# Performance work log

Measured on AMD Instinct MI355X. Metric: run time of the kernel, lower is better.

## Reference

```python
import jax, jax.numpy as jnp
import numpy as np

B, S, FC, FO = 16, 512, 24, 16
D, H, DK, FF, L = 512, 8, 64, 2048, 4
MAXPOS = 512
EPS = 1e-6


def _ln(x, scale, bias):
    mu = jnp.mean(x, axis=-1, keepdims=True)
    var = jnp.mean((x - mu) ** 2, axis=-1, keepdims=True)
    return (x - mu) * jax.lax.rsqrt(var + EPS) * scale + bias


def setup_inputs() -> dict:
    key = jax.random.key(0)
    ks = iter(jax.random.split(key, 64))
    def rn(shape, s=0.02):
        return (jax.random.normal(next(ks), shape, dtype=jnp.float32) * s)
    inp = {
        'x_cgm': jax.random.normal(next(ks), (B, S, FC), dtype=jnp.float32),
        'x_other': jax.random.normal(next(ks), (B, FO), dtype=jnp.float32),
        'cgm_W': rn((FC, D)), 'cgm_b': jnp.zeros((D,), jnp.float32),
        'rel_emb': rn((2 * MAXPOS - 1, DK)),
        'Wq': rn((L, D, H * DK)), 'bq': jnp.zeros((L, H * DK), jnp.float32),
        'Wk': rn((L, D, H * DK)), 'bk': jnp.zeros((L, H * DK), jnp.float32),
        'Wv': rn((L, D, H * DK)), 'bv': jnp.zeros((L, H * DK), jnp.float32),
        'Wo': rn((L, H * DK, D)), 'bo': jnp.zeros((L, D), jnp.float32),
        'Wg': rn((L, D, D)), 'bg': jnp.zeros((L, D), jnp.float32),
        'Wf1': rn((L, D, FF)), 'bf1': jnp.zeros((L, FF), jnp.float32),
        'Wfg': rn((L, D, FF)), 'bfg': jnp.zeros((L, FF), jnp.float32),
        'Wf2': rn((L, FF, D)), 'bf2': jnp.zeros((L, D), jnp.float32),
        'ln1_s': jnp.ones((L, D), jnp.float32), 'ln1_b': jnp.zeros((L, D), jnp.float32),
        'ln2_s': jnp.ones((L, D), jnp.float32), 'ln2_b': jnp.zeros((L, D), jnp.float32),
        'other_W': rn((FO, D)), 'other_b': jnp.zeros((D,), jnp.float32),
        'fW1': rn((2 * D, 256)), 'fb1': jnp.zeros((256,), jnp.float32),
        'fln1_s': jnp.ones((256,), jnp.float32), 'fln1_b': jnp.zeros((256,), jnp.float32),
        'fW2': rn((256, 128)), 'fb2': jnp.zeros((128,), jnp.float32),
        'fln2_s': jnp.ones((128,), jnp.float32), 'fln2_b': jnp.zeros((128,), jnp.float32),
        'fW3': rn((128, 1)), 'fb3': jnp.zeros((1,), jnp.float32),
    }
    return inp


def reference(x_cgm, x_other, cgm_W, cgm_b, rel_emb, Wq, bq, Wk, bk, Wv, bv,
              Wo, bo, Wg, bg, Wf1, bf1, Wfg, bfg, Wf2, bf2,
              ln1_s, ln1_b, ln2_s, ln2_b, other_W, other_b,
              fW1, fb1, fln1_s, fln1_b, fW2, fb2, fln2_s, fln2_b, fW3, fb3):
    x = x_cgm @ cgm_W + cgm_b  # [B,S,D]
    # relative position bias: rel_emb[i-j+MAXPOS-1] -> [S,S,DK], reduced by mean over depth
    idx = jnp.arange(S)
    pos_idx = idx[:, None] - idx[None, :] + MAXPOS - 1
    pos_bias = jnp.mean(rel_emb[pos_idx], axis=-1)  # [S,S]
    scale = jnp.sqrt(jnp.float32(DK))
    for l in range(L):
        q = (x @ Wq[l] + bq[l]).reshape(B, S, H, DK)
        k = (x @ Wk[l] + bk[l]).reshape(B, S, H, DK)
        v = (x @ Wv[l] + bv[l]).reshape(B, S, H, DK)
        scores = jnp.einsum('bqhd,bkhd->bhqk', q, k) / scale + pos_bias  # [B,H,S,S]
        probs = jax.nn.softmax(scores, axis=-1)
        ctx = jnp.einsum('bhqk,bkhd->bqhd', probs, v).reshape(B, S, H * DK)
        att = ctx @ Wo[l] + bo[l]
        gate = jax.nn.sigmoid(x @ Wg[l] + bg[l])
        x = _ln(x + gate * att, ln1_s[l], ln1_b[l])
        ff = (x @ Wf1[l] + bf1[l]) * jax.nn.sigmoid(x @ Wfg[l] + bfg[l])
        ff = ff @ Wf2[l] + bf2[l]
        x = _ln(x + ff, ln2_s[l], ln2_b[l])
    x = jnp.mean(x, axis=1)  # [B,D]
    xo = x_other @ other_W + other_b
    h = jnp.concatenate([x, xo], axis=-1)  # [B,2D]
    h = jax.nn.relu(_ln(h @ fW1 + fb1, fln1_s, fln1_b))
    h = jax.nn.relu(_ln(h @ fW2 + fb2, fln2_s, fln2_b))
    return h @ fW3 + fb3  # [B,1]
```

## Files before the change

kernel.cpp:

```cpp
#include <hip/hip_runtime.h>
#include <math.h>

constexpr int Bn = 16;
constexpr int Sn = 512;
constexpr int FCn = 24;
constexpr int FOn = 16;
constexpr int Dn = 512;
constexpr int Hn = 8;
constexpr int DKn = 64;
constexpr int FFn = 2048;
constexpr int Ln = 4;
constexpr int MAXPOSn = 512;
constexpr float EPSf = 1e-6f;

typedef __attribute__((ext_vector_type(8))) short bf16x8;
typedef __attribute__((ext_vector_type(4))) float floatx4;

__device__ __forceinline__ float sigmoidf_(float x) { return 1.0f / (1.0f + __expf(-x)); }

__device__ __forceinline__ unsigned short f2bf(float f) {
  unsigned int u = __float_as_uint(f);
  u += 0x7fffu + ((u >> 16) & 1u);
  return (unsigned short)(u >> 16);
}
__device__ __forceinline__ float b2f(unsigned short b) {
  return __uint_as_float(((unsigned int)b) << 16);
}

__device__ __forceinline__ void g2l16(const void* g, void* l) {
  __builtin_amdgcn_global_load_lds((const __attribute__((address_space(1))) void*)g,
                                   (__attribute__((address_space(3))) void*)l, 16, 0, 0);
}

__device__ __forceinline__ void st_bf16_pair(unsigned short* dst, float v, int lane) {
  unsigned int us = f2bf(v);
  unsigned int other = (unsigned int)__shfl_xor((int)us, 1);
  if (!(lane & 1)) *(unsigned int*)dst = us | (other << 16);
}

__device__ __forceinline__ float blockReduceSum(float v) {
  #pragma unroll
  for (int off = 32; off >= 1; off >>= 1) v += __shfl_xor(v, off);
  __shared__ float red[8];
  const int w = threadIdx.x >> 6;
  const int nw = blockDim.x >> 6;
  if ((threadIdx.x & 63) == 0) red[w] = v;
  __syncthreads();
  float r = 0.0f;
  for (int i = 0; i < nw; ++i) r += red[i];
  __syncthreads();
  return r;
}

__global__ __launch_bounds__(256) void wconv_kernel(
    const float* __restrict__ in, unsigned short* __restrict__ out,
    int K, int N, size_t inStride, size_t outStride) {
  __shared__ float tile[32][33];
  in += (size_t)blockIdx.z * inStride;
  out += (size_t)blockIdx.z * outStride;
  const int k0 = blockIdx.y * 32, n0 = blockIdx.x * 32;
  const int tr = threadIdx.x >> 3;
  const int tc4 = (threadIdx.x & 7) * 4;
  float4 vv = *(const float4*)&in[(size_t)(k0 + tr) * N + n0 + tc4];
  tile[tr][tc4 + 0] = vv.x; tile[tr][tc4 + 1] = vv.y;
  tile[tr][tc4 + 2] = vv.z; tile[tr][tc4 + 3] = vv.w;
  __syncthreads();
  ushort4 o4;
  o4.x = f2bf(tile[tc4 + 0][tr]); o4.y = f2bf(tile[tc4 + 1][tr]);
  o4.z = f2bf(tile[tc4 + 2][tr]); o4.w = f2bf(tile[tc4 + 3][tr]);
  *(ushort4*)&out[(size_t)(n0 + tr) * K + k0 + tc4] = o4;
}

__global__ void bcat_kernel(const float* __restrict__ bq, const float* __restrict__ bk,
                            const float* __restrict__ bv, const float* __restrict__ bg,
                            float* __restrict__ out) {
  const int t = blockIdx.x * 256 + threadIdx.x;
  const int l = t >> 11;
  const int c = t & 2047;
  float v;
  if (c < 512) v = bq[l * 512 + c];
  else if (c < 1024) v = bk[l * 512 + c - 512];
  else if (c < 1536) v = bv[l * 512 + c - 1024];
  else v = bg[l * 512 + c - 1536];
  out[t] = v;
}

__global__ __launch_bounds__(256) void embed_kernel(
    const float* __restrict__ xc, const float* __restrict__ W,
    const float* __restrict__ bias, float* __restrict__ x,
    unsigned short* __restrict__ xb) {
  const int idx = blockIdx.x * 256 + threadIdx.x;
  const int n = idx & (Dn - 1);
  const int m = idx >> 9;
  const float* xr = xc + m * FCn;
  float acc = bias[n];
  #pragma unroll
  for (int k = 0; k < FCn; ++k) acc = fmaf(xr[k], W[k * Dn + n], acc);
  x[idx] = acc;
  xb[idx] = f2bf(acc);
}

__global__ void relmean_kernel(const float* __restrict__ rel, float* __restrict__ rm) {
  const int p = blockIdx.x * blockDim.x + threadIdx.x;
  if (p >= 2 * MAXPOSn - 1) return;
  float s = 0.0f;
  #pragma unroll 8
  for (int d = 0; d < DKn; ++d) s += rel[p * DKn + d];
  rm[p] = s * (1.0f / DKn);
}

template <int EPI>
__global__ __launch_bounds__(256) void mgemm(
    const unsigned short* __restrict__ A, const unsigned short* __restrict__ Bt,
    const float* __restrict__ bias, float* __restrict__ Cf,
    unsigned short* __restrict__ Cb, unsigned short* __restrict__ Cb2,
    int Astride, int N, int Koff, int Klen, int ldc, int nt) {
  __shared__ unsigned short As[128 * 32];
  __shared__ unsigned short Bs[128 * 32];
  const int t = threadIdx.x;
  const int w = t >> 6;
  const int lane = t & 63;
  const int id = blockIdx.x;
  const int xcd = id & 7;
  const int lid = id >> 3;
  const int n0 = (lid % nt) * 128;
  const int m0 = (xcd * 8 + lid / nt) * 128;
  const int wm = (w >> 1) * 64;
  const int wn = (w & 1) * 64;
  const int lr = lane & 15;
  const int lq = lane >> 4;

  floatx4 acc[4][4];
  #pragma unroll
  for (int i = 0; i < 4; ++i)
    #pragma unroll
    for (int j = 0; j < 4; ++j) acc[i][j] = (floatx4){0.f, 0.f, 0.f, 0.f};

  const int srow = lane >> 2;
  const int schk = (lane & 3) * 8;

  for (int k0 = Koff; k0 < Koff + Klen; k0 += 32) {
    __syncthreads();
    #pragma unroll
    for (int r = 0; r < 2; ++r) {
      const int rb = (w * 2 + r) * 16;
      g2l16(&A[(size_t)(m0 + rb + srow) * Astride + k0 + schk], &As[rb * 32]);
      g2l16(&Bt[(size_t)(n0 + rb + srow) * Astride + k0 + schk], &Bs[rb * 32]);
    }
    __syncthreads();
    bf16x8 af[4], bf[4];
    #pragma unroll
    for (int i = 0; i < 4; ++i)
      af[i] = *(const bf16x8*)&As[(wm + i * 16 + lr) * 32 + lq * 8];
    #pragma unroll
    for (int j = 0; j < 4; ++j)
      bf[j] = *(const bf16x8*)&Bs[(wn + j * 16 + lr) * 32 + lq * 8];
    #pragma unroll
    for (int i = 0; i < 4; ++i)
      #pragma unroll
      for (int j = 0; j < 4; ++j)
        acc[i][j] = __builtin_amdgcn_mfma_f32_16x16x32_bf16(af[i], bf[j], acc[i][j], 0, 0, 0);
  }

  #pragma unroll
  for (int i = 0; i < 4; ++i) {
    const int row = m0 + wm + i * 16 + lq * 4;
    #pragma unroll
    for (int j = 0; j < 4; ++j) {
      const int col = n0 + wn + j * 16 + lr;
      const int colp = col & ~1;
      #pragma unroll
      for (int r = 0; r < 4; ++r) {
        if (EPI == 0) {
          Cf[(size_t)(row + r) * ldc + col] = acc[i][j][r] + bias[col];
        } else if (EPI == 5) {
          const size_t idx = (size_t)(row + r) * ldc + col;
          Cf[idx] += acc[i][j][r];
        } else if (EPI == 3) {
          st_bf16_pair(&Cb[(size_t)(row + r) * ldc + colp], acc[i][j][r] + bias[col], lane);
        } else if (EPI == 4) {
          const float va = acc[i][j][r] + bias[col];
          if (col < 1536)
            st_bf16_pair(&Cb[(size_t)(row + r) * 1536 + colp], va, lane);
          else
            st_bf16_pair(&Cb2[(size_t)(row + r) * 512 + (colp - 1536)], sigmoidf_(va), lane);
        }
      }
    }
  }
}

__global__ __launch_bounds__(256) void ffgemm(
    const unsigned short* __restrict__ A, const unsigned short* __restrict__ B1t,
    const unsigned short* __restrict__ B2t, const float* __restrict__ b1,
    const float* __restrict__ b2, unsigned short* __restrict__ C, int K) {
  __shared__ unsigned short As[128 * 32];
  __shared__ unsigned short B1s[64 * 32];
  __shared__ unsigned short B2s[64 * 32];
  const int t = threadIdx.x;
  const int w = t >> 6;
  const int lane = t & 63;
  const int id = blockIdx.x;
  const int xcd = id & 7;
  const int lid = id >> 3;
  const int n0 = (lid & 31) * 64;
  const int m0 = (xcd * 8 + (lid >> 5)) * 128;
  const int wm = (w >> 1) * 64;
  const int wn = (w & 1) * 32;
  const int lr = lane & 15;
  const int lq = lane >> 4;

  floatx4 a1[4][2], a2[4][2];
  #pragma unroll
  for (int i = 0; i < 4; ++i)
    #pragma unroll
    for (int j = 0; j < 2; ++j) {
      a1[i][j] = (floatx4){0.f, 0.f, 0.f, 0.f};
      a2[i][j] = (floatx4){0.f, 0.f, 0.f, 0.f};
    }

  const int srow = lane >> 2;
  const int schk = (lane & 3) * 8;

  for (int k0 = 0; k0 < K; k0 += 32) {
    __syncthreads();
    g2l16(&A[(size_t)(m0 + w * 32 + srow) * K + k0 + schk], &As[(w * 32) * 32]);
    g2l16(&A[(size_t)(m0 + w * 32 + 16 + srow) * K + k0 + schk], &As[(w * 32 + 16) * 32]);
    g2l16(&B1t[(size_t)(n0 + w * 16 + srow) * K + k0 + schk], &B1s[(w * 16) * 32]);
    g2l16(&B2t[(size_t)(n0 + w * 16 + srow) * K + k0 + schk], &B2s[(w * 16) * 32]);
    __syncthreads();
    bf16x8 af[4], f1[2], f2[2];
    #pragma unroll
    for (int i = 0; i < 4; ++i)
      af[i] = *(const bf16x8*)&As[(wm + i * 16 + lr) * 32 + lq * 8];
    #pragma unroll
    for (int j = 0; j < 2; ++j) {
      f1[j] = *(const bf16x8*)&B1s[(wn + j * 16 + lr) * 32 + lq * 8];
      f2[j] = *(const bf16x8*)&B2s[(wn + j * 16 + lr) * 32 + lq * 8];
    }
    #pragma unroll
    for (int i = 0; i < 4; ++i)
      #pragma unroll
      for (int j = 0; j < 2; ++j) {
        a1[i][j] = __builtin_amdgcn_mfma_f32_16x16x32_bf16(af[i], f1[j], a1[i][j], 0, 0, 0);
        a2[i][j] = __builtin_amdgcn_mfma_f32_16x16x32_bf16(af[i], f2[j], a2[i][j], 0, 0, 0);
      }
  }

  #pragma unroll
  for (int i = 0; i < 4; ++i) {
    const int row = m0 + wm + i * 16 + lq * 4;
    #pragma unroll
    for (int j = 0; j < 2; ++j) {
      const int col = n0 + wn + j * 16 + lr;
      const int colp = col & ~1;
      const float bb1 = b1[col], bb2 = b2[col];
      #pragma unroll
      for (int r = 0; r < 4; ++r) {
        const float f = (a1[i][j][r] + bb1) * sigmoidf_(a2[i][j][r] + bb2);
        st_bf16_pair(&C[(size_t)(row + r) * 2048 + colp], f, lane);
      }
    }
  }
}

__global__ __launch_bounds__(256) void attn_kernel(
    const unsigned short* __restrict__ qkv, const float* __restrict__ rm,
    unsigned short* __restrict__ ctx) {
  __shared__ unsigned short Ks[64 * 72];
  __shared__ unsigned short Vt[64 * 72];
  __shared__ unsigned short Pw[4][16 * 72];
  __shared__ float rml[576];
  const int t = threadIdx.x;
  const int w = t >> 6;
  const int lane = t & 63;
  const int lr = lane & 15;
  const int lq = lane >> 4;
  const int bid = blockIdx.x;
  const int b = bid & 15;
  const int h = (bid >> 4) & 7;
  const int qt = bid >> 7;
  const int q0 = qt * 64;
  const size_t rowb = (size_t)b * Sn * 1536;

  for (int i = t; i < 576; i += 256) rml[i] = rm[q0 + i];

  bf16x8 aq0, aq1;
  {
    const unsigned short* qp = &qkv[rowb + (size_t)(q0 + w * 16 + lr) * 1536 + h * 64 + lq * 8];
    aq0 = *(const bf16x8*)qp;
    aq1 = *(const bf16x8*)(qp + 32);
  }

  floatx4 o_acc[4];
  #pragma unroll
  for (int i = 0; i < 4; ++i) o_acc[i] = (floatx4){0.f, 0.f, 0.f, 0.f};
  float m_old[4] = {-1e30f, -1e30f, -1e30f, -1e30f};
  float l_sum[4] = {0.f, 0.f, 0.f, 0.f};

  const int skey = t >> 2;
  const int schk = (t & 3) * 16;
  const int vkp = t >> 4;
  const int vd4 = (t & 15) * 4;

  for (int kc = 0; kc < 8; ++kc) {
    __syncthreads();
    {
      const unsigned short* gk = &qkv[rowb + (size_t)(kc * 64 + skey) * 1536 + 512 + h * 64 + schk];
      *(bf16x8*)&Ks[skey * 72 + schk] = *(const bf16x8*)gk;
      *(bf16x8*)&Ks[skey * 72 + schk + 8] = *(const bf16x8*)(gk + 8);
    }
    #pragma unroll
    for (int pass = 0; pass < 2; ++pass) {
      const int kp = vkp + pass * 16;
      const unsigned short* gv = &qkv[rowb + (size_t)(kc * 64 + kp * 2) * 1536 + 1024 + h * 64 + vd4];
      ushort4 v0 = *(const ushort4*)gv;
      ushort4 v1 = *(const ushort4*)(gv + 1536);
      *(ushort2*)&Vt[(vd4 + 0) * 72 + kp * 2] = make_ushort2(v0.x, v1.x);
      *(ushort2*)&Vt[(vd4 + 1) * 72 + kp * 2] = make_ushort2(v0.y, v1.y);
      *(ushort2*)&Vt[(vd4 + 2) * 72 + kp * 2] = make_ushort2(v0.z, v1.z);
      *(ushort2*)&Vt[(vd4 + 3) * 72 + kp * 2] = make_ushort2(v0.w, v1.w);
    }
    __syncthreads();

    floatx4 s_acc[4];
    #pragma unroll
    for (int j = 0; j < 4; ++j) {
      bf16x8 b0 = *(const bf16x8*)&Ks[(j * 16 + lr) * 72 + lq * 8];
      bf16x8 b1 = *(const bf16x8*)&Ks[(j * 16 + lr) * 72 + 32 + lq * 8];
      s_acc[j] = __builtin_amdgcn_mfma_f32_16x16x32_bf16(aq0, b0, (floatx4){0.f, 0.f, 0.f, 0.f}, 0, 0, 0);
      s_acc[j] = __builtin_amdgcn_mfma_f32_16x16x32_bf16(aq1, b1, s_acc[j], 0, 0, 0);
    }

    float mloc[4] = {-1e30f, -1e30f, -1e30f, -1e30f};
    #pragma unroll
    for (int j = 0; j < 4; ++j) {
      const int key = kc * 64 + j * 16 + lr;
      #pragma unroll
      for (int r = 0; r < 4; ++r) {
        const float sv = s_acc[j][r] * 0.125f + rml[(w * 16 + lq * 4 + r) + 511 - key];
        s_acc[j][r] = sv;
        mloc[r] = fmaxf(mloc[r], sv);
      }
    }
    #pragma unroll
    for (int off = 1; off <= 8; off <<= 1)
      #pragma unroll
      for (int r = 0; r < 4; ++r) mloc[r] = fmaxf(mloc[r], __shfl_xor(mloc[r], off));

    float alpha[4], rsum[4];
    #pragma unroll
    for (int r = 0; r < 4; ++r) {
      const float mnew = fmaxf(m_old[r], mloc[r]);
      alpha[r] = __expf(m_old[r] - mnew);
      m_old[r] = mnew;
      rsum[r] = 0.f;
    }
    #pragma unroll
    for (int j = 0; j < 4; ++j)
      #pragma unroll
      for (int r = 0; r < 4; ++r) {
        const float p = __expf(s_acc[j][r] - m_old[r]);
        rsum[r] += p;
        Pw[w][(lq * 4 + r) * 72 + j * 16 + lr] = f2bf(p);
      }
    #pragma unroll
    for (int off = 1; off <= 8; off <<= 1)
      #pragma unroll
      for (int r = 0; r < 4; ++r) rsum[r] += __shfl_xor(rsum[r], off);
    #pragma unroll
    for (int r = 0; r < 4; ++r) l_sum[r] = l_sum[r] * alpha[r] + rsum[r];
    #pragma unroll
    for (int i = 0; i < 4; ++i)
      #pragma unroll
      for (int r = 0; r < 4; ++r) o_acc[i][r] *= alpha[r];

    bf16x8 ap0 = *(const bf16x8*)&Pw[w][lr * 72 + lq * 8];
    bf16x8 ap1 = *(const bf16x8*)&Pw[w][lr * 72 + 32 + lq * 8];
    #pragma unroll
    for (int i = 0; i < 4; ++i) {
      bf16x8 v0 = *(const bf16x8*)&Vt[(i * 16 + lr) * 72 + lq * 8];
      bf16x8 v1 = *(const bf16x8*)&Vt[(i * 16 + lr) * 72 + 32 + lq * 8];
      o_acc[i] = __builtin_amdgcn_mfma_f32_16x16x32_bf16(ap0, v0, o_acc[i], 0, 0, 0);
      o_acc[i] = __builtin_amdgcn_mfma_f32_16x16x32_bf16(ap1, v1, o_acc[i], 0, 0, 0);
    }
  }

  float rinv[4];
  #pragma unroll
  for (int r = 0; r < 4; ++r) rinv[r] = 1.0f / l_sum[r];
  #pragma unroll
  for (int i = 0; i < 4; ++i)
    #pragma unroll
    for (int r = 0; r < 4; ++r) {
      const int q = q0 + w * 16 + lq * 4 + r;
      ctx[((size_t)(b * Sn + q)) * Dn + h * 64 + i * 16 + lr] = f2bf(o_acc[i][r] * rinv[r]);
    }
}

__global__ __launch_bounds__(256) void ln_res1_kernel(
    float* __restrict__ x, unsigned short* __restrict__ xb,
    const unsigned short* __restrict__ att, const unsigned short* __restrict__ gate,
    const float* __restrict__ s, const float* __restrict__ bsh) {
  const int row = blockIdx.x;
  const int t = threadIdx.x;
  const size_t base = (size_t)row * Dn;
  float y0 = x[base + t] + b2f(att[base + t]) * b2f(gate[base + t]);
  float y1 = x[base + t + 256] + b2f(att[base + t + 256]) * b2f(gate[base + t + 256]);
  const float mu = blockReduceSum(y0 + y1) * (1.0f / Dn);
  const float d0 = y0 - mu, d1 = y1 - mu;
  const float var = blockReduceSum(d0 * d0 + d1 * d1) * (1.0f / Dn);
  const float rstd = rsqrtf(var + EPSf);
  const float o0 = d0 * rstd * s[t] + bsh[t];
  const float o1 = d1 * rstd * s[t + 256] + bsh[t + 256];
  x[base + t] = o0;
  x[base + t + 256] = o1;
  xb[base + t] = f2bf(o0);
  xb[base + t + 256] = f2bf(o1);
}

__global__ __launch_bounds__(256) void ln_res2_kernel(
    float* __restrict__ x, unsigned short* __restrict__ xb,
    const float* __restrict__ add, const float* __restrict__ s,
    const float* __restrict__ bsh) {
  const int row = blockIdx.x;
  const int t = threadIdx.x;
  const size_t base = (size_t)row * Dn;
  float y0 = x[base + t] + add[base + t];
  float y1 = x[base + t + 256] + add[base + t + 256];
  const float mu = blockReduceSum(y0 + y1) * (1.0f / Dn);
  const float d0 = y0 - mu, d1 = y1 - mu;
  const float var = blockReduceSum(d0 * d0 + d1 * d1) * (1.0f / Dn);
  const float rstd = rsqrtf(var + EPSf);
  const float o0 = d0 * rstd * s[t] + bsh[t];
  const float o1 = d1 * rstd * s[t + 256] + bsh[t + 256];
  x[base + t] = o0;
  x[base + t + 256] = o1;
  xb[base + t] = f2bf(o0);
  xb[base + t + 256] = f2bf(o1);
}

__global__ __launch_bounds__(256) void mp_part_kernel(const float* __restrict__ x,
                                                      float* __restrict__ part) {
  const int b = blockIdx.x, sc = blockIdx.y;
  const int t = threadIdx.x;
  float s0 = 0.f, s1 = 0.f;
  for (int si = sc * 64; si < sc * 64 + 64; ++si) {
    s0 += x[((size_t)(b * Sn + si)) * Dn + t];
    s1 += x[((size_t)(b * Sn + si)) * Dn + t + 256];
  }
  part[(size_t)(b * 8 + sc) * 512 + t] = s0;
  part[(size_t)(b * 8 + sc) * 512 + t + 256] = s1;
}

__global__ __launch_bounds__(256) void mp_comb_kernel(const float* __restrict__ part,
                                                      float* __restrict__ h) {
  const int idx = blockIdx.x * 256 + threadIdx.x;
  const int b = idx >> 9, d = idx & 511;
  float s = 0.f;
  #pragma unroll
  for (int i = 0; i < 8; ++i) s += part[(size_t)(b * 8 + i) * 512 + d];
  h[b * 1024 + d] = s * (1.0f / Sn);
}

__global__ __launch_bounds__(256) void xo_kernel(const float* __restrict__ xo,
                                                 const float* __restrict__ W,
                                                 const float* __restrict__ bias,
                                                 float* __restrict__ h) {
  const int idx = blockIdx.x * 256 + threadIdx.x;
  const int b = idx >> 9;
  const int n = idx & 511;
  float acc = bias[n];
  #pragma unroll
  for (int k = 0; k < FOn; ++k) acc = fmaf(xo[b * FOn + k], W[k * Dn + n], acc);
  h[b * 1024 + 512 + n] = acc;
}

__global__ __launch_bounds__(256) void f1a_kernel(
    const float* __restrict__ h, const float* __restrict__ W,
    float* __restrict__ part) {
  const int b = blockIdx.x, kq = blockIdx.y;
  const int n = threadIdx.x;
  const float* hr = h + b * 1024 + kq * 128;
  const float* Wp = W + (size_t)(kq * 128) * 256 + n;
  float acc = 0.f;
  #pragma unroll 8
  for (int k = 0; k < 128; ++k) acc = fmaf(hr[k], Wp[(size_t)k * 256], acc);
  part[(size_t)(b * 8 + kq) * 256 + n] = acc;
}

__global__ __launch_bounds__(256) void f1b_kernel(
    const float* __restrict__ part, const float* __restrict__ bias,
    const float* __restrict__ s, const float* __restrict__ bt,
    float* __restrict__ o) {
  const int b = blockIdx.x;
  const int n = threadIdx.x;
  float acc = bias[n];
  #pragma unroll
  for (int i = 0; i < 8; ++i) acc += part[(size_t)(b * 8 + i) * 256 + n];
  const float mu = blockReduceSum(acc) * (1.0f / 256.0f);
  const float d = acc - mu;
  const float var = blockReduceSum(d * d) * (1.0f / 256.0f);
  const float y = d * rsqrtf(var + EPSf) * s[n] + bt[n];
  o[b * 256 + n] = fmaxf(y, 0.0f);
}

__global__ __launch_bounds__(512) void f2_kernel(
    const float* __restrict__ h1, const float* __restrict__ W,
    const float* __restrict__ bias, const float* __restrict__ s,
    const float* __restrict__ bt, float* __restrict__ o) {
  __shared__ float h1row[256];
  __shared__ float partial[4][128];
  const int b = blockIdx.x;
  const int t = threadIdx.x;
  if (t < 256) h1row[t] = h1[b * 256 + t];
  __syncthreads();
  const int n = t & 127, ks = t >> 7;
  float acc = 0.f;
  #pragma unroll 8
  for (int k = ks * 64; k < ks * 64 + 64; ++k) acc = fmaf(h1row[k], W[k * 128 + n], acc);
  partial[ks][n] = acc;
  __syncthreads();
  float v = 0.f;
  if (t < 128)
    v = partial[0][t] + partial[1][t] + partial[2][t] + partial[3][t] + bias[t];
  const float mu = blockReduceSum(t < 128 ? v : 0.f) * (1.0f / 128.0f);
  const float d = (t < 128) ? v - mu : 0.f;
  const float var = blockReduceSum(d * d) * (1.0f / 128.0f);
  if (t < 128) o[b * 128 + t] = fmaxf(d * rsqrtf(var + EPSf) * s[t] + bt[t], 0.0f);
}

__global__ __launch_bounds__(128) void f3_kernel(const float* __restrict__ h2,
                                                 const float* __restrict__ W,
                                                 const float* __restrict__ bias,
                                                 float* __restrict__ o) {
  const int b = blockIdx.x;
  const int t = threadIdx.x;
  float v = h2[b * 128 + t] * W[t];
  v = blockReduceSum(v);
  if (t == 0) o[b] = v + bias[0];
}

extern "C" void kernel_launch(void* const* d_in, const int* in_sizes, int n_in,
                              void* d_out, int out_size, void* d_ws, size_t ws_size,
                              hipStream_t stream) {
  (void)in_sizes; (void)n_in; (void)out_size; (void)ws_size;
  const float* x_cgm  = (const float*)d_in[0];
  const float* x_other= (const float*)d_in[1];
  const float* cgm_W  = (const float*)d_in[2];
  const float* cgm_b  = (const float*)d_in[3];
  const float* rel_emb= (const float*)d_in[4];
  const float* Wq = (const float*)d_in[5];
  const float* bq = (const float*)d_in[6];
  const float* Wk = (const float*)d_in[7];
  const float* bk = (const float*)d_in[8];
  const float* Wv = (const float*)d_in[9];
  const float* bv = (const float*)d_in[10];
  const float* Wo = (const float*)d_in[11];
  const float* bo = (const float*)d_in[12];
  const float* Wg = (const float*)d_in[13];
  const float* bg = (const float*)d_in[14];
  const float* Wf1 = (const float*)d_in[15];
  const float* bf1 = (const float*)d_in[16];
  const float* Wfg = (const float*)d_in[17];
  const float* bfg = (const float*)d_in[18];
  const float* Wf2 = (const float*)d_in[19];
  const float* bf2 = (const float*)d_in[20];
  const float* ln1_s = (const float*)d_in[21];
  const float* ln1_b = (const float*)d_in[22];
  const float* ln2_s = (const float*)d_in[23];
  const float* ln2_b = (const float*)d_in[24];
  const float* other_W = (const float*)d_in[25];
  const float* other_b = (const float*)d_in[26];
  const float* fW1 = (const float*)d_in[27];
  const float* fb1 = (const float*)d_in[28];
  const float* fln1_s = (const float*)d_in[29];
  const float* fln1_b = (const float*)d_in[30];
  const float* fW2 = (const float*)d_in[31];
  const float* fb2 = (const float*)d_in[32];
  const float* fln2_s = (const float*)d_in[33];
  const float* fln2_b = (const float*)d_in[34];
  const float* fW3 = (const float*)d_in[35];
  const float* fb3 = (const float*)d_in[36];
  float* out = (float*)d_out;

  char* p = (char*)d_ws;
  auto alloc = [&](size_t bytes) { char* r = p; p += (bytes + 255) & ~(size_t)255; return r; };
  float*          X      = (float*)alloc((size_t)8192 * 512 * 4);
  unsigned short* Xb     = (unsigned short*)alloc((size_t)8192 * 512 * 2);
  unsigned short* QKVb   = (unsigned short*)alloc((size_t)8192 * 1536 * 2);
  unsigned short* CTXb   = (unsigned short*)alloc((size_t)8192 * 512 * 2);
  char*           R      = alloc((size_t)8192 * 2048 * 2);
  unsigned short* ATTb   = (unsigned short*)R;
  unsigned short* GATEb  = (unsigned short*)(R + (size_t)8192 * 512 * 2);
  unsigned short* FFBh   = (unsigned short*)R;
  float*          CTXo   = (float*)QKVb;
  unsigned short* Wqkvgt = (unsigned short*)alloc((size_t)4 * 2048 * 512 * 2);
  unsigned short* Wot    = (unsigned short*)alloc((size_t)4 * 512 * 512 * 2);
  unsigned short* Wf1t   = (unsigned short*)alloc((size_t)4 * 2048 * 512 * 2);
  unsigned short* Wfgt   = (unsigned short*)alloc((size_t)4 * 2048 * 512 * 2);
  unsigned short* Wf2t   = (unsigned short*)alloc((size_t)4 * 512 * 2048 * 2);
  float*          bqkvg  = (float*)alloc((size_t)4 * 2048 * 4);
  float*          RMb    = (float*)alloc(1024 * 4);
  float*          Hb     = (float*)alloc(16 * 1024 * 4);
  float*          H1b    = (float*)alloc(16 * 256 * 4);
  float*          H2b    = (float*)alloc(16 * 128 * 4);
  float*          MPP    = (float*)alloc((size_t)16 * 8 * 512 * 4);
  float*          F1P    = (float*)alloc((size_t)16 * 8 * 256 * 4);

  wconv_kernel<<<dim3(16, 16, 4), 256, 0, stream>>>(Wq, Wqkvgt + (size_t)0 * 512, 512, 512,
                                                    (size_t)512 * 512, (size_t)2048 * 512);
  wconv_kernel<<<dim3(16, 16, 4), 256, 0, stream>>>(Wk, Wqkvgt + (size_t)512 * 512, 512, 512,
                                                    (size_t)512 * 512, (size_t)2048 * 512);
  wconv_kernel<<<dim3(16, 16, 4), 256, 0, stream>>>(Wv, Wqkvgt + (size_t)1024 * 512, 512, 512,
                                                    (size_t)512 * 512, (size_t)2048 * 512);
  wconv_kernel<<<dim3(16, 16, 4), 256, 0, stream>>>(Wg, Wqkvgt + (size_t)1536 * 512, 512, 512,
                                                    (size_t)512 * 512, (size_t)2048 * 512);
  wconv_kernel<<<dim3(16, 16, 4), 256, 0, stream>>>(Wo, Wot, 512, 512,
                                                    (size_t)512 * 512, (size_t)512 * 512);
  wconv_kernel<<<dim3(64, 16, 4), 256, 0, stream>>>(Wf1, Wf1t, 512, 2048,
                                                    (size_t)512 * 2048, (size_t)2048 * 512);
  wconv_kernel<<<dim3(64, 16, 4), 256, 0, stream>>>(Wfg, Wfgt, 512, 2048,
                                                    (size_t)512 * 2048, (size_t)2048 * 512);
  wconv_kernel<<<dim3(16, 64, 4), 256, 0, stream>>>(Wf2, Wf2t, 2048, 512,
                                                    (size_t)2048 * 512, (size_t)512 * 2048);
  bcat_kernel<<<dim3(32), 256, 0, stream>>>(bq, bk, bv, bg, bqkvg);

  embed_kernel<<<dim3(16384), dim3(256), 0, stream>>>(x_cgm, cgm_W, cgm_b, X, Xb);
  relmean_kernel<<<dim3(4), dim3(256), 0, stream>>>(rel_emb, RMb);

  for (int l = 0; l < Ln; ++l) {
    const size_t bof = (size_t)l * Dn;
    mgemm<4><<<dim3(1024), 256, 0, stream>>>(Xb, Wqkvgt + (size_t)l * 2048 * 512,
                                             bqkvg + (size_t)l * 2048, nullptr, QKVb, GATEb,
                                             512, 2048, 0, 512, 0, 16);
    attn_kernel<<<dim3(1024), dim3(256), 0, stream>>>(QKVb, RMb, CTXb);
    mgemm<3><<<dim3(256), 256, 0, stream>>>(CTXb, Wot + (size_t)l * 512 * 512,
                                            bo + bof, nullptr, ATTb, nullptr,
                                            512, 512, 0, 512, 512, 4);
    ln_res1_kernel<<<dim3(8192), 256, 0, stream>>>(X, Xb, ATTb, GATEb, ln1_s + bof, ln1_b + bof);
    ffgemm<<<dim3(2048), 256, 0, stream>>>(Xb, Wf1t + (size_t)l * 2048 * 512,
                                           Wfgt + (size_t)l * 2048 * 512,
                                           bf1 + (size_t)l * FFn, bfg + (size_t)l * FFn,
                                           FFBh, 512);
    mgemm<0><<<dim3(256), 256, 0, stream>>>(FFBh, Wf2t + (size_t)l * 512 * 2048,
                                            bf2 + bof, CTXo, nullptr, nullptr,
                                            2048, 512, 0, 1024, 512, 4);
    mgemm<5><<<dim3(256), 256, 0, stream>>>(FFBh, Wf2t + (size_t)l * 512 * 2048,
                                            nullptr, CTXo, nullptr, nullptr,
                                            2048, 512, 1024, 1024, 512, 4);
    ln_res2_kernel<<<dim3(8192), 256, 0, stream>>>(X, Xb, CTXo, ln2_s + bof, ln2_b + bof);
  }

  mp_part_kernel<<<dim3(16, 8), 256, 0, stream>>>(X, MPP);
  mp_comb_kernel<<<dim3(32), 256, 0, stream>>>(MPP, Hb);
  xo_kernel<<<dim3(32), dim3(256), 0, stream>>>(x_other, other_W, other_b, Hb);
  f1a_kernel<<<dim3(16, 8), 256, 0, stream>>>(Hb, fW1, F1P);
  f1b_kernel<<<dim3(16), 256, 0, stream>>>(F1P, fb1, fln1_s, fln1_b, H1b);
  f2_kernel<<<dim3(16), 512, 0, stream>>>(H1b, fW2, fb2, fln2_s, fln2_b, H2b);
  f3_kernel<<<dim3(16), 128, 0, stream>>>(H2b, fW3, fb3, out);
}
```

Before: 1.242 ms.

## Double GEMM K-step with XOR-swizzled LDS, wave-per-row layernorm, fuse tail kernels

The mgemm and ffgemm kernels now stage a K-slice of 64 per iteration instead of 32, using an XOR-swizzled shared-memory layout to avoid bank conflicts. This halves the number of barrier pairs per GEMM at the cost of twice the LDS use. The layernorm-residual kernels now handle one row per wave with vectorized loads and shuffle-only reductions, so no block-level reductions are needed. The small head kernels (mean-pool combine plus the other-features projection, and the f1b/f2/f3 MLP tail) are merged into fewer launches.

New measurement: 1.213 ms. 2.4% less time.

```diff
diff --git a/kernel.cpp b/kernel.cpp
--- a/kernel.cpp
+++ b/kernel.cpp
@@ -38,9 +38,14 @@
   if (!(lane & 1)) *(unsigned int*)dst = us | (other << 16);
 }
 
+__device__ __forceinline__ float waveReduceSum(float v) {
+  #pragma unroll
+  for (int off = 32; off >= 1; off >>= 1) v += __shfl_xor(v, off);
+  return v;
+}
+
 __device__ __forceinline__ float blockReduceSum(float v) {
-  #pragma unroll
-  for (int off = 32; off >= 1; off >>= 1) v += __shfl_xor(v, off);
+  v = waveReduceSum(v);
   __shared__ float red[8];
   const int w = threadIdx.x >> 6;
   const int nw = blockDim.x >> 6;
@@ -115,8 +120,8 @@
     const float* __restrict__ bias, float* __restrict__ Cf,
     unsigned short* __restrict__ Cb, unsigned short* __restrict__ Cb2,
     int Astride, int N, int Koff, int Klen, int ldc, int nt) {
-  __shared__ unsigned short As[128 * 32];
-  __shared__ unsigned short Bs[128 * 32];
+  __shared__ unsigned short As[128 * 64];
+  __shared__ unsigned short Bs[128 * 64];
   const int t = threadIdx.x;
   const int w = t >> 6;
   const int lane = t & 63;
@@ -136,30 +141,37 @@
     #pragma unroll
     for (int j = 0; j < 4; ++j) acc[i][j] = (floatx4){0.f, 0.f, 0.f, 0.f};
 
-  const int srow = lane >> 2;
-  const int schk = (lane & 3) * 8;
-
-  for (int k0 = Koff; k0 < Koff + Klen; k0 += 32) {
+  const int srow = lane >> 3;
+  const int sg = ((lane & 7) ^ srow) * 8;
+  const int r7 = lr & 7;
+  const int p0 = (lq ^ r7) * 8;
+  const int p1 = ((4 + lq) ^ r7) * 8;
+
+  for (int k0 = Koff; k0 < Koff + Klen; k0 += 64) {
     __syncthreads();
     #pragma unroll
-    for (int r = 0; r < 2; ++r) {
-      const int rb = (w * 2 + r) * 16;
-      g2l16(&A[(size_t)(m0 + rb + srow) * Astride + k0 + schk], &As[rb * 32]);
-      g2l16(&Bt[(size_t)(n0 + rb + srow) * Astride + k0 + schk], &Bs[rb * 32]);
+    for (int r = 0; r < 4; ++r) {
+      const int rb = (w * 4 + r) * 8;
+      g2l16(&A[(size_t)(m0 + rb + srow) * Astride + k0 + sg], &As[rb * 64]);
+      g2l16(&Bt[(size_t)(n0 + rb + srow) * Astride + k0 + sg], &Bs[rb * 64]);
     }
     __syncthreads();
-    bf16x8 af[4], bf[4];
-    #pragma unroll
-    for (int i = 0; i < 4; ++i)
-      af[i] = *(const bf16x8*)&As[(wm + i * 16 + lr) * 32 + lq * 8];
-    #pragma unroll
-    for (int j = 0; j < 4; ++j)
-      bf[j] = *(const bf16x8*)&Bs[(wn + j * 16 + lr) * 32 + lq * 8];
-    #pragma unroll
-    for (int i = 0; i < 4; ++i)
+    #pragma unroll
+    for (int s = 0; s < 2; ++s) {
+      const int ps = s ? p1 : p0;
+      bf16x8 af[4], bf[4];
+      #pragma unroll
+      for (int i = 0; i < 4; ++i)
+        af[i] = *(const bf16x8*)&As[(wm + i * 16 + lr) * 64 + ps];
       #pragma unroll
       for (int j = 0; j < 4; ++j)
-        acc[i][j] = __builtin_amdgcn_mfma_f32_16x16x32_bf16(af[i], bf[j], acc[i][j], 0, 0, 0);
+        bf[j] = *(const bf16x8*)&Bs[(wn + j * 16 + lr) * 64 + ps];
+      #pragma unroll
+      for (int i = 0; i < 4; ++i)
+        #pragma unroll
+        for (int j = 0; j < 4; ++j)
+          acc[i][j] = __builtin_amdgcn_mfma_f32_16x16x32_bf16(af[i], bf[j], acc[i][j], 0, 0, 0);
+    }
   }
 
   #pragma unroll
@@ -194,9 +206,9 @@
     const unsigned short* __restrict__ A, const unsigned short* __restrict__ B1t,
     const unsigned short* __restrict__ B2t, const float* __restrict__ b1,
     const float* __restrict__ b2, unsigned short* __restrict__ C, int K) {
-  __shared__ unsigned short As[128 * 32];
-  __shared__ unsigned short B1s[64 * 32];
-  __shared__ unsigned short B2s[64 * 32];
+  __shared__ unsigned short As[128 * 64];
+  __shared__ unsigned short B1s[64 * 64];
+  __shared__ unsigned short B2s[64 * 64];
   const int t = threadIdx.x;
   const int w = t >> 6;
   const int lane = t & 63;
@@ -219,32 +231,46 @@
       a2[i][j] = (floatx4){0.f, 0.f, 0.f, 0.f};
     }
 
-  const int srow = lane >> 2;
-  const int schk = (lane & 3) * 8;
-
-  for (int k0 = 0; k0 < K; k0 += 32) {
+  const int srow = lane >> 3;
+  const int sg = ((lane & 7) ^ srow) * 8;
+  const int r7 = lr & 7;
+  const int p0 = (lq ^ r7) * 8;
+  const int p1 = ((4 + lq) ^ r7) * 8;
+
+  for (int k0 = 0; k0 < K; k0 += 64) {
     __syncthreads();
-    g2l16(&A[(size_t)(m0 + w * 32 + srow) * K + k0 + schk], &As[(w * 32) * 32]);
-    g2l16(&A[(size_t)(m0 + w * 32 + 16 + srow) * K + k0 + schk], &As[(w * 32 + 16) * 32]);
-    g2l16(&B1t[(size_t)(n0 + w * 16 + srow) * K + k0 + schk], &B1s[(w * 16) * 32]);
-    g2l16(&B2t[(size_t)(n0 + w * 16 + srow) * K + k0 + schk], &B2s[(w * 16) * 32]);
+    #pragma unroll
+    for (int r = 0; r < 4; ++r) {
+      const int rb = (w * 4 + r) * 8;
+      g2l16(&A[(size_t)(m0 + rb + srow) * K + k0 + sg], &As[rb * 64]);
+    }
+    #pragma unroll
+    for (int r = 0; r < 2; ++r) {
+      const int rb = (w * 2 + r) * 8;
+      g2l16(&B1t[(size_t)(n0 + rb + srow) * K + k0 + sg], &B1s[rb * 64]);
+      g2l16(&B2t[(size_t)(n0 + rb + srow) * K + k0 + sg], &B2s[rb * 64]);
+    }
     __syncthreads();
-    bf16x8 af[4], f1[2], f2[2];
-    #pragma unroll
-    for (int i = 0; i < 4; ++i)
-      af[i] = *(const bf16x8*)&As[(wm + i * 16 + lr) * 32 + lq * 8];
-    #pragma unroll
-    for (int j = 0; j < 2; ++j) {
-      f1[j] = *(const bf16x8*)&B1s[(wn + j * 16 + lr) * 32 + lq * 8];
-      f2[j] = *(const bf16x8*)&B2s[(wn + j * 16 + lr) * 32 + lq * 8];
-    }
-    #pragma unroll
-    for (int i = 0; i < 4; ++i)
+    #pragma unroll
+    for (int s = 0; s < 2; ++s) {
+      const int ps = s ? p1 : p0;
+      bf16x8 af[4], f1[2], f2[2];
+      #pragma unroll
+      for (int i = 0; i < 4; ++i)
+        af[i] = *(const bf16x8*)&As[(wm + i * 16 + lr) * 64 + ps];
       #pragma unroll
       for (int j = 0; j < 2; ++j) {
-        a1[i][j] = __builtin_amdgcn_mfma_f32_16x16x32_bf16(af[i], f1[j], a1[i][j], 0, 0, 0);
-        a2[i][j] = __builtin_amdgcn_mfma_f32_16x16x32_bf16(af[i], f2[j], a2[i][j], 0, 0, 0);
+        f1[j] = *(const bf16x8*)&B1s[(wn + j * 16 + lr) * 64 + ps];
+        f2[j] = *(const bf16x8*)&B2s[(wn + j * 16 + lr) * 64 + ps];
       }
+      #pragma unroll
+      for (int i = 0; i < 4; ++i)
+        #pragma unroll
+        for (int j = 0; j < 2; ++j) {
+          a1[i][j] = __builtin_amdgcn_mfma_f32_16x16x32_bf16(af[i], f1[j], a1[i][j], 0, 0, 0);
+          a2[i][j] = __builtin_amdgcn_mfma_f32_16x16x32_bf16(af[i], f2[j], a2[i][j], 0, 0, 0);
+        }
+    }
   }
 
   #pragma unroll
@@ -402,42 +428,85 @@
     float* __restrict__ x, unsigned short* __restrict__ xb,
     const unsigned short* __restrict__ att, const unsigned short* __restrict__ gate,
     const float* __restrict__ s, const float* __restrict__ bsh) {
-  const int row = blockIdx.x;
-  const int t = threadIdx.x;
+  const int w = threadIdx.x >> 6, lane = threadIdx.x & 63;
+  const int row = blockIdx.x * 4 + w;
   const size_t base = (size_t)row * Dn;
-  float y0 = x[base + t] + b2f(att[base + t]) * b2f(gate[base + t]);
-  float y1 = x[base + t + 256] + b2f(att[base + t + 256]) * b2f(gate[base + t + 256]);
-  const float mu = blockReduceSum(y0 + y1) * (1.0f / Dn);
-  const float d0 = y0 - mu, d1 = y1 - mu;
-  const float var = blockReduceSum(d0 * d0 + d1 * d1) * (1.0f / Dn);
-  const float rstd = rsqrtf(var + EPSf);
-  const float o0 = d0 * rstd * s[t] + bsh[t];
-  const float o1 = d1 * rstd * s[t + 256] + bsh[t + 256];
-  x[base + t] = o0;
-  x[base + t + 256] = o1;
-  xb[base + t] = f2bf(o0);
-  xb[base + t + 256] = f2bf(o1);
+  const int c = lane * 4;
+  float4 xv0 = *(const float4*)&x[base + c];
+  float4 xv1 = *(const float4*)&x[base + c + 256];
+  ushort4 a0 = *(const ushort4*)&att[base + c];
+  ushort4 a1 = *(const ushort4*)&att[base + c + 256];
+  ushort4 g0 = *(const ushort4*)&gate[base + c];
+  ushort4 g1 = *(const ushort4*)&gate[base + c + 256];
+  float y[8];
+  y[0] = xv0.x + b2f(a0.x) * b2f(g0.x);
+  y[1] = xv0.y + b2f(a0.y) * b2f(g0.y);
+  y[2] = xv0.z + b2f(a0.z) * b2f(g0.z);
+  y[3] = xv0.w + b2f(a0.w) * b2f(g0.w);
+  y[4] = xv1.x + b2f(a1.x) * b2f(g1.x);
+  y[5] = xv1.y + b2f(a1.y) * b2f(g1.y);
+  y[6] = xv1.z + b2f(a1.z) * b2f(g1.z);
+  y[7] = xv1.w + b2f(a1.w) * b2f(g1.w);
+  float sum = 0.f;
+  #pragma unroll
+  for (int i = 0; i < 8; ++i) sum += y[i];
+  const float mu = waveReduceSum(sum) * (1.0f / Dn);
+  float vs = 0.f;
+  #pragma unroll
+  for (int i = 0; i < 8; ++i) { y[i] -= mu; vs += y[i] * y[i]; }
+  const float rstd = rsqrtf(waveReduceSum(vs) * (1.0f / Dn) + EPSf);
+  float4 s0 = *(const float4*)&s[c], s1 = *(const float4*)&s[c + 256];
+  float4 b0 = *(const float4*)&bsh[c], b1 = *(const float4*)&bsh[c + 256];
+  float4 o0, o1;
+  o0.x = y[0] * rstd * s0.x + b0.x; o0.y = y[1] * rstd * s0.y + b0.y;
+  o0.z = y[2] * rstd * s0.z + b0.z; o0.w = y[3] * rstd * s0.w + b0.w;
+  o1.x = y[4] * rstd * s1.x + b1.x; o1.y = y[5] * rstd * s1.y + b1.y;
+  o1.z = y[6] * rstd * s1.z + b1.z; o1.w = y[7] * rstd * s1.w + b1.w;
+  *(float4*)&x[base + c] = o0;
+  *(float4*)&x[base + c + 256] = o1;
+  ushort4 ob0, ob1;
+  ob0.x = f2bf(o0.x); ob0.y = f2bf(o0.y); ob0.z = f2bf(o0.z); ob0.w = f2bf(o0.w);
+  ob1.x = f2bf(o1.x); ob1.y = f2bf(o1.y); ob1.z = f2bf(o1.z); ob1.w = f2bf(o1.w);
+  *(ushort4*)&xb[base + c] = ob0;
+  *(ushort4*)&xb[base + c + 256] = ob1;
 }
 
 __global__ __launch_bounds__(256) void ln_res2_kernel(
     float* __restrict__ x, unsigned short* __restrict__ xb,
     const float* __restrict__ add, const float* __restrict__ s,
     const float* __restrict__ bsh) {
-  const int row = blockIdx.x;
-  const int t = threadIdx.x;
+  const int w = threadIdx.x >> 6, lane = threadIdx.x & 63;
+  const int row = blockIdx.x * 4 + w;
   const size_t base = (size_t)row * Dn;
-  float y0 = x[base + t] + add[base + t];
-  float y1 = x[base + t + 256] + add[base + t + 256];
-  const float mu = blockReduceSum(y0 + y1) * (1.0f / Dn);
-  const float d0 = y0 - mu, d1 = y1 - mu;
-  const float var = blockReduceSum(d0 * d0 + d1 * d1) * (1.0f / Dn);
-  const float rstd = rsqrtf(var + EPSf);
-  const float o0 = d0 * rstd * s[t] + bsh[t];
-  const float o1 = d1 * rstd * s[t + 256] + bsh[t + 256];
-  x[base + t] = o0;
-  x[base + t + 256] = o1;
-  xb[base + t] = f2bf(o0);
-  xb[base + t + 256] = f2bf(o1);
+  const int c = lane * 4;
+  float4 xv0 = *(const float4*)&x[base + c];
+  float4 xv1 = *(const float4*)&x[base + c + 256];
+  float4 a0 = *(const float4*)&add[base + c];
+  float4 a1 = *(const float4*)&add[base + c + 256];
+  float y[8] = {xv0.x + a0.x, xv0.y + a0.y, xv0.z + a0.z, xv0.w + a0.w,
+                xv1.x + a1.x, xv1.y + a1.y, xv1.z + a1.z, xv1.w + a1.w};
+  float sum = 0.f;
+  #pragma unroll
+  for (int i = 0; i < 8; ++i) sum += y[i];
+  const float mu = waveReduceSum(sum) * (1.0f / Dn);
+  float vs = 0.f;
+  #pragma unroll
+  for (int i = 0; i < 8; ++i) { y[i] -= mu; vs += y[i] * y[i]; }
+  const float rstd = rsqrtf(waveReduceSum(vs) * (1.0f / Dn) + EPSf);
+  float4 s0 = *(const float4*)&s[c], s1 = *(const float4*)&s[c + 256];
+  float4 b0 = *(const float4*)&bsh[c], b1 = *(const float4*)&bsh[c + 256];
+  float4 o0, o1;
+  o0.x = y[0] * rstd * s0.x + b0.x; o0.y = y[1] * rstd * s0.y + b0.y;
+  o0.z = y[2] * rstd * s0.z + b0.z; o0.w = y[3] * rstd * s0.w + b0.w;
+  o1.x = y[4] * rstd * s1.x + b1.x; o1.y = y[5] * rstd * s1.y + b1.y;
+  o1.z = y[6] * rstd * s1.z + b1.z; o1.w = y[7] * rstd * s1.w + b1.w;
+  *(float4*)&x[base + c] = o0;
+  *(float4*)&x[base + c + 256] = o1;
+  ushort4 ob0, ob1;
+  ob0.x = f2bf(o0.x); ob0.y = f2bf(o0.y); ob0.z = f2bf(o0.z); ob0.w = f2bf(o0.w);
+  ob1.x = f2bf(o1.x); ob1.y = f2bf(o1.y); ob1.z = f2bf(o1.z); ob1.w = f2bf(o1.w);
+  *(ushort4*)&xb[base + c] = ob0;
+  *(ushort4*)&xb[base + c + 256] = ob1;
 }
 
 __global__ __launch_bounds__(256) void mp_part_kernel(const float* __restrict__ x,
@@ -453,27 +522,20 @@
   part[(size_t)(b * 8 + sc) * 512 + t + 256] = s1;
 }
 
-__global__ __launch_bounds__(256) void mp_comb_kernel(const float* __restrict__ part,
-                                                      float* __restrict__ h) {
+__global__ __launch_bounds__(256) void mp_comb_xo_kernel(
+    const float* __restrict__ part, const float* __restrict__ xo,
+    const float* __restrict__ oW, const float* __restrict__ ob,
+    float* __restrict__ h) {
   const int idx = blockIdx.x * 256 + threadIdx.x;
   const int b = idx >> 9, d = idx & 511;
   float s = 0.f;
   #pragma unroll
   for (int i = 0; i < 8; ++i) s += part[(size_t)(b * 8 + i) * 512 + d];
   h[b * 1024 + d] = s * (1.0f / Sn);
-}
-
-__global__ __launch_bounds__(256) void xo_kernel(const float* __restrict__ xo,
-                                                 const float* __restrict__ W,
-                                                 const float* __restrict__ bias,
-                                                 float* __restrict__ h) {
-  const int idx = blockIdx.x * 256 + threadIdx.x;
-  const int b = idx >> 9;
-  const int n = idx & 511;
-  float acc = bias[n];
-  #pragma unroll
-  for (int k = 0; k < FOn; ++k) acc = fmaf(xo[b * FOn + k], W[k * Dn + n], acc);
-  h[b * 1024 + 512 + n] = acc;
+  float acc = ob[d];
+  #pragma unroll
+  for (int k = 0; k < FOn; ++k) acc = fmaf(xo[b * FOn + k], oW[k * Dn + d], acc);
+  h[b * 1024 + 512 + d] = acc;
 }
 
 __global__ __launch_bounds__(256) void f1a_kernel(
@@ -489,56 +551,40 @@
   part[(size_t)(b * 8 + kq) * 256 + n] = acc;
 }
 
-__global__ __launch_bounds__(256) void f1b_kernel(
-    const float* __restrict__ part, const float* __restrict__ bias,
-    const float* __restrict__ s, const float* __restrict__ bt,
-    float* __restrict__ o) {
-  const int b = blockIdx.x;
-  const int n = threadIdx.x;
-  float acc = bias[n];
-  #pragma unroll
-  for (int i = 0; i < 8; ++i) acc += part[(size_t)(b * 8 + i) * 256 + n];
-  const float mu = blockReduceSum(acc) * (1.0f / 256.0f);
-  const float d = acc - mu;
-  const float var = blockReduceSum(d * d) * (1.0f / 256.0f);
-  const float y = d * rsqrtf(var + EPSf) * s[n] + bt[n];
-  o[b * 256 + n] = fmaxf(y, 0.0f);
-}
-
-__global__ __launch_bounds__(512) void f2_kernel(
-    const float* __restrict__ h1, const float* __restrict__ W,
-    const float* __restrict__ bias, const float* __restrict__ s,
-    const float* __restrict__ bt, float* __restrict__ o) {
-  __shared__ float h1row[256];
-  __shared__ float partial[4][128];
+__global__ __launch_bounds__(256) void tail_kernel(
+    const float* __restrict__ part, const float* __restrict__ fb1,
+    const float* __restrict__ fln1_s, const float* __restrict__ fln1_b,
+    const float* __restrict__ fW2, const float* __restrict__ fb2,
+    const float* __restrict__ fln2_s, const float* __restrict__ fln2_b,
+    const float* __restrict__ fW3, const float* __restrict__ fb3,
+    float* __restrict__ out) {
+  __shared__ float h1[256];
   const int b = blockIdx.x;
   const int t = threadIdx.x;
-  if (t < 256) h1row[t] = h1[b * 256 + t];
+  float acc = fb1[t];
+  #pragma unroll
+  for (int i = 0; i < 8; ++i) acc += part[(size_t)(b * 8 + i) * 256 + t];
+  float mu = blockReduceSum(acc) * (1.0f / 256.0f);
+  float d = acc - mu;
+  float var = blockReduceSum(d * d) * (1.0f / 256.0f);
+  h1[t] = fmaxf(d * rsqrtf(var + EPSf) * fln1_s[t] + fln1_b[t], 0.0f);
   __syncthreads();
-  const int n = t & 127, ks = t >> 7;
-  float acc = 0.f;
-  #pragma unroll 8
-  for (int k = ks * 64; k < ks * 64 + 64; ++k) acc = fmaf(h1row[k], W[k * 128 + n], acc);
-  partial[ks][n] = acc;
-  __syncthreads();
+  float acc2 = 0.f;
+  if (t < 128) {
+    #pragma unroll 8
+    for (int k = 0; k < 256; ++k) acc2 = fmaf(h1[k], fW2[k * 128 + t], acc2);
+    acc2 += fb2[t];
+  }
+  mu = blockReduceSum(t < 128 ? acc2 : 0.f) * (1.0f / 128.0f);
+  d = (t < 128) ? acc2 - mu : 0.f;
+  var = blockReduceSum(d * d) * (1.0f / 128.0f);
   float v = 0.f;
-  if (t < 128)
-    v = partial[0][t] + partial[1][t] + partial[2][t] + partial[3][t] + bias[t];
-  const float mu = blockReduceSum(t < 128 ? v : 0.f) * (1.0f / 128.0f);
-  const float d = (t < 128) ? v - mu : 0.f;
-  const float var = blockReduceSum(d * d) * (1.0f / 128.0f);
-  if (t < 128) o[b * 128 + t] = fmaxf(d * rsqrtf(var + EPSf) * s[t] + bt[t], 0.0f);
-}
-
-__global__ __launch_bounds__(128) void f3_kernel(const float* __restrict__ h2,
-                                                 const float* __restrict__ W,
-                                                 const float* __restrict__ bias,
-                                                 float* __restrict__ o) {
-  const int b = blockIdx.x;
-  const int t = threadIdx.x;
-  float v = h2[b * 128 + t] * W[t];
+  if (t < 128) {
+    const float h2v = fmaxf(d * rsqrtf(var + EPSf) * fln2_s[t] + fln2_b[t], 0.0f);
+    v = h2v * fW3[t];
+  }
   v = blockReduceSum(v);
-  if (t == 0) o[b] = v + bias[0];
+  if (t == 0) out[b] = v + fb3[0];
 }
 
 extern "C" void kernel_launch(void* const* d_in, const int* in_sizes, int n_in,
@@ -603,8 +649,6 @@
   float*          bqkvg  = (float*)alloc((size_t)4 * 2048 * 4);
   float*          RMb    = (float*)alloc(1024 * 4);
   float*          Hb     = (float*)alloc(16 * 1024 * 4);
-  float*          H1b    = (float*)alloc(16 * 256 * 4);
-  float*          H2b    = (float*)alloc(16 * 128 * 4);
   float*          MPP    = (float*)alloc((size_t)16 * 8 * 512 * 4);
   float*          F1P    = (float*)alloc((size_t)16 * 8 * 256 * 4);
 
@@ -638,7 +682,7 @@
     mgemm<3><<<dim3(256), 256, 0, stream>>>(CTXb, Wot + (size_t)l * 512 * 512,
                                             bo + bof, nullptr, ATTb, nullptr,
                                             512, 512, 0, 512, 512, 4);
-    ln_res1_kernel<<<dim3(8192), 256, 0, stream>>>(X, Xb, ATTb, GATEb, ln1_s + bof, ln1_b + bof);
+    ln_res1_kernel<<<dim3(2048), 256, 0, stream>>>(X, Xb, ATTb, GATEb, ln1_s + bof, ln1_b + bof);
     ffgemm<<<dim3(2048), 256, 0, stream>>>(Xb, Wf1t + (size_t)l * 2048 * 512,
                                            Wfgt + (size_t)l * 2048 * 512,
                                            bf1 + (size_t)l * FFn, bfg + (size_t)l * FFn,
@@ -649,14 +693,12 @@
     mgemm<5><<<dim3(256), 256, 0, stream>>>(FFBh, Wf2t + (size_t)l * 512 * 2048,
                                             nullptr, CTXo, nullptr, nullptr,
                                             2048, 512, 1024, 1024, 512, 4);
-    ln_res2_kernel<<<dim3(8192), 256, 0, stream>>>(X, Xb, CTXo, ln2_s + bof, ln2_b + bof);
+    ln_res2_kernel<<<dim3(2048), 256, 0, stream>>>(X, Xb, CTXo, ln2_s + bof, ln2_b + bof);
   }
 
   mp_part_kernel<<<dim3(16, 8), 256, 0, stream>>>(X, MPP);
-  mp_comb_kernel<<<dim3(32), 256, 0, stream>>>(MPP, Hb);
-  xo_kernel<<<dim3(32), dim3(256), 0, stream>>>(x_other, other_W, other_b, Hb);
+  mp_comb_xo_kernel<<<dim3(32), 256, 0, stream>>>(MPP, x_other, other_W, other_b, Hb);
   f1a_kernel<<<dim3(16, 8), 256, 0, stream>>>(Hb, fW1, F1P);
-  f1b_kernel<<<dim3(16), 256, 0, stream>>>(F1P, fb1, fln1_s, fln1_b, H1b);
-  f2_kernel<<<dim3(16), 512, 0, stream>>>(H1b, fW2, fb2, fln2_s, fln2_b, H2b);
-  f3_kernel<<<dim3(16), 128, 0, stream>>>(H2b, fW3, fb3, out);
-}
+  tail_kernel<<<dim3(16), 256, 0, stream>>>(F1P, fb1, fln1_s, fln1_b,
+                                            fW2, fb2, fln2_s, fln2_b, fW3, fb3, out);
+}
```
